# Kernel tuning notes

Hardware: AMD Instinct MI355X
Metric: run time of the kernel (lower is better)

## Reference

```python
import jax, jax.numpy as jnp
import numpy as np

EMBED = 2048
HQ = 32
HKV = 8
HD = EMBED // HQ          # 64
G = HQ // HKV             # 4 q heads per kv head
SCALE = 1.0 / np.sqrt(EMBED)  # module uses 1/sqrt(embed_dim), not head_dim
B, S = 4, 2048


def setup_inputs() -> dict:
    key = jax.random.key(0)
    ks = jax.random.split(key, 10)
    x = jax.random.normal(ks[0], (B, S, EMBED), dtype=jnp.float32)
    # RoPE tables: theta=10000, angles[t, i] = t / theta^(2i/HD)
    inv_freq = 1.0 / (10000.0 ** (jnp.arange(0, HD, 2, dtype=jnp.float32) / HD))  # [HD/2]
    angles = jnp.arange(S, dtype=jnp.float32)[:, None] * inv_freq[None, :]        # [S, HD/2]
    freqs_cos = jnp.cos(angles)
    freqs_sin = jnp.sin(angles)
    s = 0.02
    wq_w = jax.random.normal(ks[1], (EMBED, EMBED), jnp.float32) * s
    wq_b = jnp.zeros((EMBED,), jnp.float32)
    wk_w = jax.random.normal(ks[2], (HKV * HD, EMBED), jnp.float32) * s
    wk_b = jnp.zeros((HKV * HD,), jnp.float32)
    wv_w = jax.random.normal(ks[3], (HKV * HD, EMBED), jnp.float32) * s
    wv_b = jnp.zeros((HKV * HD,), jnp.float32)
    wo_w = jax.random.normal(ks[4], (EMBED, EMBED), jnp.float32) * s
    wo_b = jnp.zeros((EMBED,), jnp.float32)
    return dict(x=x, freqs_cos=freqs_cos, freqs_sin=freqs_sin,
                wq_w=wq_w, wq_b=wq_b, wk_w=wk_w, wk_b=wk_b,
                wv_w=wv_w, wv_b=wv_b, wo_w=wo_w, wo_b=wo_b)


def _rope(t, cos, sin):
    # t: [B, S, H, HD]; cos/sin: [S, HD/2] -> broadcast [1, S, 1, HD/2]
    tr = t[..., 0::2]
    ti = t[..., 1::2]
    c = cos[None, :, None, :]
    s = sin[None, :, None, :]
    out_r = tr * c - ti * s
    out_i = tr * s + ti * c
    # interleave back to [..., HD]
    return jnp.stack([out_r, out_i], axis=-1).reshape(t.shape)


def _forward(x, freqs_cos, freqs_sin, wq_w, wq_b, wk_w, wk_b, wv_w, wv_b, wo_w, wo_b):
    b, s, _ = x.shape
    q = (x @ wq_w.T + wq_b).reshape(b, s, HQ, HD)
    k = (x @ wk_w.T + wk_b).reshape(b, s, HKV, HD)
    v = (x @ wv_w.T + wv_b).reshape(b, s, HKV, HD)
    q = _rope(q, freqs_cos, freqs_sin)
    k = _rope(k, freqs_cos, freqs_sin)
    # GQA: group q heads as [HKV, G] instead of repeat_interleave'ing k/v
    qg = q.reshape(b, s, HKV, G, HD)
    scores = jnp.einsum('bqhgd,bkhd->bhgqk', qg, k) * SCALE  # [B,HKV,G,S,S]
    causal = jnp.tril(jnp.ones((s, s), dtype=bool))
    scores = jnp.where(causal, scores, jnp.finfo(scores.dtype).min)
    p = jax.nn.softmax(scores, axis=-1)
    o = jnp.einsum('bhgqk,bkhd->bqhgd', p, v).reshape(b, s, EMBED)
    return o @ wo_w.T + wo_b


def reference(x, freqs_cos, freqs_sin, wq_w, wq_b, wk_w, wk_b, wv_w, wv_b, wo_w, wo_b):
    return _forward(x, freqs_cos, freqs_sin, wq_w, wq_b, wk_w, wk_b,
                    wv_w, wv_b, wo_w, wo_b)
```

## Files before the change

### kernel.cpp

```cpp
#include <hip/hip_runtime.h>
#include <stdint.h>

typedef unsigned short u16;
typedef __attribute__((ext_vector_type(8))) short bf16x8;
typedef __attribute__((ext_vector_type(4))) float f32x4;

#define MFMA_BF16(a,b,c) __builtin_amdgcn_mfma_f32_16x16x32_bf16((a),(b),(c),0,0,0)

__device__ inline u16 f2bf(float f) {
  uint32_t u = __builtin_bit_cast(uint32_t, f);
  u = (u + 0x7FFFu + ((u >> 16) & 1u)) >> 16;
  return (u16)u;
}
__device__ inline float bf2f(u16 h) {
  uint32_t u = ((uint32_t)h) << 16;
  return __builtin_bit_cast(float, u);
}

__global__ __launch_bounds__(256) void cvt_kernel(const float* __restrict__ src,
                                                  u16* __restrict__ dst, int n4) {
  int i = blockIdx.x * 256 + threadIdx.x;
  if (i >= n4) return;
  float4 v = reinterpret_cast<const float4*>(src)[i];
  uint2 o;
  o.x = (uint32_t)f2bf(v.x) | ((uint32_t)f2bf(v.y) << 16);
  o.y = (uint32_t)f2bf(v.z) | ((uint32_t)f2bf(v.w) << 16);
  reinterpret_cast<uint2*>(dst)[i] = o;
}

template<typename OutT>
__global__ __launch_bounds__(256) void gemm_bt(
    const u16* __restrict__ A, const u16* __restrict__ B,
    const float* __restrict__ bias, OutT* __restrict__ C,
    int M, int N, int K)
{
  constexpr int LDT = 72;
  __shared__ u16 As[128 * LDT];
  __shared__ u16 Bs[128 * LDT];
  const int bm = blockIdx.y, bn = blockIdx.x;
  const int tid = threadIdx.x;
  const int lane = tid & 63;
  const int wv = tid >> 6;
  const int wm = wv >> 1, wn = wv & 1;
  const int g = lane >> 4, qn = lane & 15;

  f32x4 acc[4][4];
  #pragma unroll
  for (int i = 0; i < 4; ++i)
    #pragma unroll
    for (int j = 0; j < 4; ++j) acc[i][j] = (f32x4){0.f, 0.f, 0.f, 0.f};

  const u16* Ab = A + (size_t)bm * 128 * K;
  const u16* Bb = B + (size_t)bn * 128 * K;

  for (int kt = 0; kt < K; kt += 64) {
    __syncthreads();
    #pragma unroll
    for (int i = 0; i < 4; ++i) {
      int u = tid + 256 * i;
      int row = u >> 3, c = u & 7;
      uint4 va = *reinterpret_cast<const uint4*>(Ab + (size_t)row * K + kt + c * 8);
      *reinterpret_cast<uint4*>(As + row * LDT + c * 8) = va;
      uint4 vb = *reinterpret_cast<const uint4*>(Bb + (size_t)row * K + kt + c * 8);
      *reinterpret_cast<uint4*>(Bs + row * LDT + c * 8) = vb;
    }
    __syncthreads();
    #pragma unroll
    for (int ks = 0; ks < 2; ++ks) {
      bf16x8 af[4], bfr[4];
      #pragma unroll
      for (int mi = 0; mi < 4; ++mi)
        af[mi] = *reinterpret_cast<const bf16x8*>(As + (wm * 64 + mi * 16 + qn) * LDT + g * 8 + ks * 32);
      #pragma unroll
      for (int ni = 0; ni < 4; ++ni)
        bfr[ni] = *reinterpret_cast<const bf16x8*>(Bs + (wn * 64 + ni * 16 + qn) * LDT + g * 8 + ks * 32);
      #pragma unroll
      for (int mi = 0; mi < 4; ++mi)
        #pragma unroll
        for (int ni = 0; ni < 4; ++ni)
          acc[mi][ni] = MFMA_BF16(af[mi], bfr[ni], acc[mi][ni]);
    }
  }
  #pragma unroll
  for (int ni = 0; ni < 4; ++ni) {
    int col = bn * 128 + wn * 64 + ni * 16 + qn;
    float bs = bias[col];
    #pragma unroll
    for (int mi = 0; mi < 4; ++mi) {
      #pragma unroll
      for (int r = 0; r < 4; ++r) {
        int row = bm * 128 + wm * 64 + mi * 16 + g * 4 + r;
        float v = acc[mi][ni][r] + bs;
        if constexpr (sizeof(OutT) == 2) C[(size_t)row * N + col] = (OutT)f2bf(v);
        else                             C[(size_t)row * N + col] = v;
      }
    }
  }
}

__global__ __launch_bounds__(256) void rope_kernel(
    u16* __restrict__ T, const float* __restrict__ cosT, const float* __restrict__ sinT,
    int heads8, int n8)
{
  int i = blockIdx.x * 256 + threadIdx.x;
  if (i >= n8) return;
  int tok = i / heads8;
  int r = i - tok * heads8;
  int d0 = (r & 7) * 8;
  int s = tok & 2047;
  uint4 v = reinterpret_cast<uint4*>(T)[i];
  u16* e = reinterpret_cast<u16*>(&v);
  float4 c = *reinterpret_cast<const float4*>(cosT + s * 32 + d0 / 2);
  float4 sn = *reinterpret_cast<const float4*>(sinT + s * 32 + d0 / 2);
  float cc[4] = {c.x, c.y, c.z, c.w}, ss[4] = {sn.x, sn.y, sn.z, sn.w};
  #pragma unroll
  for (int j = 0; j < 4; ++j) {
    float tr = bf2f(e[2 * j]), ti = bf2f(e[2 * j + 1]);
    e[2 * j]     = f2bf(tr * cc[j] - ti * ss[j]);
    e[2 * j + 1] = f2bf(tr * ss[j] + ti * cc[j]);
  }
  reinterpret_cast<uint4*>(T)[i] = v;
}

__global__ __launch_bounds__(256) void attn_kernel(
    const u16* __restrict__ Q, const u16* __restrict__ Kb,
    const u16* __restrict__ Vb, u16* __restrict__ O)
{
  constexpr int LDK = 72;
  constexpr float SCALE = 0.02209708691207961f;
  __shared__ u16 Kl[64 * LDK];
  __shared__ u16 Vt[64 * LDK];
  __shared__ u16 Pl[4][16 * LDK];
  const int qt = blockIdx.x, hq = blockIdx.y, b = blockIdx.z;
  const int kvh = hq >> 2;
  const int tid = threadIdx.x, lane = tid & 63, w = tid >> 6;
  const int g = lane >> 4, qn = lane & 15;
  const int q_g = qt * 64 + w * 16 + qn;

  const u16* qrow = Q + ((size_t)(b * 2048 + q_g) * 2048 + hq * 64);
  bf16x8 qf[2];
  qf[0] = *reinterpret_cast<const bf16x8*>(qrow + g * 8);
  qf[1] = *reinterpret_cast<const bf16x8*>(qrow + g * 8 + 32);

  float m = -1e30f, l = 0.f;
  f32x4 oa[4];
  #pragma unroll
  for (int i = 0; i < 4; ++i) oa[i] = (f32x4){0.f, 0.f, 0.f, 0.f};

  const u16* Kbase = Kb + ((size_t)b * 2048 * 512 + kvh * 64);
  const u16* Vbase = Vb + ((size_t)b * 2048 * 512 + kvh * 64);

  const int nkt = qt + 1;
  for (int kt = 0; kt < nkt; ++kt) {
    __syncthreads();
    #pragma unroll
    for (int i = 0; i < 2; ++i) {
      int u = tid + 256 * i;
      int row = u >> 3, c = u & 7;
      uint4 v = *reinterpret_cast<const uint4*>(Kbase + (size_t)(kt * 64 + row) * 512 + c * 8);
      *reinterpret_cast<uint4*>(Kl + row * LDK + c * 8) = v;
    }
    #pragma unroll
    for (int i = 0; i < 2; ++i) {
      int u = tid + 256 * i;
      int rc = u >> 6, d = u & 63;
      uint4 pack;
      u16* tmp = reinterpret_cast<u16*>(&pack);
      #pragma unroll
      for (int j = 0; j < 8; ++j)
        tmp[j] = Vbase[(size_t)(kt * 64 + rc * 8 + j) * 512 + d];
      *reinterpret_cast<uint4*>(Vt + d * LDK + rc * 8) = pack;
    }
    __syncthreads();
    f32x4 st[4];
    #pragma unroll
    for (int cf = 0; cf < 4; ++cf) st[cf] = (f32x4){0.f, 0.f, 0.f, 0.f};
    #pragma unroll
    for (int ks = 0; ks < 2; ++ks) {
      #pragma unroll
      for (int cf = 0; cf < 4; ++cf) {
        bf16x8 kf = *reinterpret_cast<const bf16x8*>(Kl + (cf * 16 + qn) * LDK + g * 8 + ks * 32);
        st[cf] = MFMA_BF16(kf, qf[ks], st[cf]);
      }
    }
    float pv[16];
    float tmax = -1e30f;
    #pragma unroll
    for (int cf = 0; cf < 4; ++cf) {
      #pragma unroll
      for (int r = 0; r < 4; ++r) {
        int kp = kt * 64 + cf * 16 + g * 4 + r;
        float s = st[cf][r] * SCALE;
        if (kp > q_g) s = -1e30f;
        pv[cf * 4 + r] = s;
        tmax = fmaxf(tmax, s);
      }
    }
    tmax = fmaxf(tmax, __shfl_xor(tmax, 16));
    tmax = fmaxf(tmax, __shfl_xor(tmax, 32));
    float mnew = fmaxf(m, tmax);
    float fac = __expf(m - mnew);
    float lsum = 0.f;
    #pragma unroll
    for (int i = 0; i < 16; ++i) { float p = __expf(pv[i] - mnew); pv[i] = p; lsum += p; }
    lsum += __shfl_xor(lsum, 16);
    lsum += __shfl_xor(lsum, 32);
    l = l * fac + lsum;
    m = mnew;
    #pragma unroll
    for (int r = 0; r < 4; ++r) {
      float fr = __shfl(fac, (lane & 48) | (g * 4 + r));
      #pragma unroll
      for (int df = 0; df < 4; ++df) oa[df][r] *= fr;
    }
    u16* Pw = Pl[w];
    #pragma unroll
    for (int cf = 0; cf < 4; ++cf) {
      #pragma unroll
      for (int h = 0; h < 2; ++h) {
        uint32_t pk = (uint32_t)f2bf(pv[cf * 4 + 2 * h]) | ((uint32_t)f2bf(pv[cf * 4 + 2 * h + 1]) << 16);
        *reinterpret_cast<uint32_t*>(Pw + qn * LDK + cf * 16 + g * 4 + 2 * h) = pk;
      }
    }
    __syncthreads();
    #pragma unroll
    for (int ks = 0; ks < 2; ++ks) {
      bf16x8 pa = *reinterpret_cast<const bf16x8*>(Pw + qn * LDK + g * 8 + ks * 32);
      #pragma unroll
      for (int df = 0; df < 4; ++df) {
        bf16x8 vf = *reinterpret_cast<const bf16x8*>(Vt + (df * 16 + qn) * LDK + g * 8 + ks * 32);
        oa[df] = MFMA_BF16(pa, vf, oa[df]);
      }
    }
  }
  #pragma unroll
  for (int r = 0; r < 4; ++r) {
    float lr = __shfl(l, (lane & 48) | (g * 4 + r));
    float inv = 1.f / lr;
    int row_g = qt * 64 + w * 16 + g * 4 + r;
    u16* orow = O + ((size_t)(b * 2048 + row_g) * 2048 + hq * 64);
    #pragma unroll
    for (int df = 0; df < 4; ++df)
      orow[df * 16 + qn] = f2bf(oa[df][r] * inv);
  }
}

extern "C" void kernel_launch(void* const* d_in, const int* in_sizes, int n_in,
                              void* d_out, int out_size, void* d_ws, size_t ws_size,
                              hipStream_t stream) {
  const float* x    = (const float*)d_in[0];
  const float* fc   = (const float*)d_in[1];
  const float* fs   = (const float*)d_in[2];
  const float* wq_w = (const float*)d_in[3];
  const float* wq_b = (const float*)d_in[4];
  const float* wk_w = (const float*)d_in[5];
  const float* wk_b = (const float*)d_in[6];
  const float* wv_w = (const float*)d_in[7];
  const float* wv_b = (const float*)d_in[8];
  const float* wo_w = (const float*)d_in[9];
  const float* wo_b = (const float*)d_in[10];
  float* out = (float*)d_out;
  char* ws = (char*)d_ws;

  const size_t NEEDED = 96468992;
  if (ws_size < NEEDED) return;

  u16* x_bf  = (u16*)(ws);
  u16* Qb    = (u16*)(ws + 33554432);
  u16* Kb    = (u16*)(ws + 67108864);
  u16* Vb    = (u16*)(ws + 75497472);
  u16* Wbuf  = (u16*)(ws + 83886080);
  u16* wk_bf = (u16*)(ws + 92274688);
  u16* wv_bf = (u16*)(ws + 94371840);
  u16* Ob    = x_bf;

  cvt_kernel<<<16384, 256, 0, stream>>>(x,    x_bf, 4194304);
  cvt_kernel<<< 4096, 256, 0, stream>>>(wq_w, Wbuf, 1048576);
  cvt_kernel<<< 1024, 256, 0, stream>>>(wk_w, wk_bf, 262144);
  cvt_kernel<<< 1024, 256, 0, stream>>>(wv_w, wv_bf, 262144);

  gemm_bt<u16><<<dim3(16, 64), 256, 0, stream>>>(x_bf, Wbuf,  wq_b, Qb, 8192, 2048, 2048);
  gemm_bt<u16><<<dim3( 4, 64), 256, 0, stream>>>(x_bf, wk_bf, wk_b, Kb, 8192,  512, 2048);
  gemm_bt<u16><<<dim3( 4, 64), 256, 0, stream>>>(x_bf, wv_bf, wv_b, Vb, 8192,  512, 2048);

  cvt_kernel<<< 4096, 256, 0, stream>>>(wo_w, Wbuf, 1048576);

  rope_kernel<<<8192, 256, 0, stream>>>(Qb, fc, fs, 256, 2097152);
  rope_kernel<<<2048, 256, 0, stream>>>(Kb, fc, fs,  64,  524288);

  attn_kernel<<<dim3(32, 32, 4), 256, 0, stream>>>(Qb, Kb, Vb, Ob);

  gemm_bt<float><<<dim3(16, 64), 256, 0, stream>>>(Ob, Wbuf, wo_b, out, 8192, 2048, 2048);
}
```

Before: 773.1 us.

## Double-buffer attention K/V with async LDS loads, swizzling and causal tile skipping

The attention kernel now double-buffers K and V tiles. It prefetches the next tile with global_load_lds for K and register-staged loads for V while computing the current one, which removes one barrier per iteration. LDS padding is replaced by XOR swizzling, Q is prescaled by the softmax scale, and on the diagonal tile each wave skips fully masked column fragments. The GEMM also switches to direct global-to-LDS loads with an unpadded layout. That layout may cause LDS bank conflicts in the GEMM fragment reads, and prescaling Q in bf16 adds rounding error.

```diff
diff --git a/kernel.cpp b/kernel.cpp
--- a/kernel.cpp
+++ b/kernel.cpp
@@ -6,6 +6,10 @@
 typedef __attribute__((ext_vector_type(4))) float f32x4;
 
 #define MFMA_BF16(a,b,c) __builtin_amdgcn_mfma_f32_16x16x32_bf16((a),(b),(c),0,0,0)
+
+#define GLOAD_LDS16(g, l) \
+  __builtin_amdgcn_global_load_lds((const __attribute__((address_space(1))) void*)(g), \
+                                   (__attribute__((address_space(3))) void*)(l), 16, 0, 0)
 
 __device__ inline u16 f2bf(float f) {
   uint32_t u = __builtin_bit_cast(uint32_t, f);
@@ -34,9 +38,8 @@
     const float* __restrict__ bias, OutT* __restrict__ C,
     int M, int N, int K)
 {
-  constexpr int LDT = 72;
-  __shared__ u16 As[128 * LDT];
-  __shared__ u16 Bs[128 * LDT];
+  __shared__ u16 As[128 * 64];
+  __shared__ u16 Bs[128 * 64];
   const int bm = blockIdx.y, bn = blockIdx.x;
   const int tid = threadIdx.x;
   const int lane = tid & 63;
@@ -52,17 +55,16 @@
 
   const u16* Ab = A + (size_t)bm * 128 * K;
   const u16* Bb = B + (size_t)bn * 128 * K;
+  const int lr = lane >> 3, lc = lane & 7;
 
   for (int kt = 0; kt < K; kt += 64) {
     __syncthreads();
     #pragma unroll
     for (int i = 0; i < 4; ++i) {
-      int u = tid + 256 * i;
-      int row = u >> 3, c = u & 7;
-      uint4 va = *reinterpret_cast<const uint4*>(Ab + (size_t)row * K + kt + c * 8);
-      *reinterpret_cast<uint4*>(As + row * LDT + c * 8) = va;
-      uint4 vb = *reinterpret_cast<const uint4*>(Bb + (size_t)row * K + kt + c * 8);
-      *reinterpret_cast<uint4*>(Bs + row * LDT + c * 8) = vb;
+      int r0 = wv * 32 + i * 8;
+      size_t goff = (size_t)(r0 + lr) * K + kt + lc * 8;
+      GLOAD_LDS16(Ab + goff, As + r0 * 64);
+      GLOAD_LDS16(Bb + goff, Bs + r0 * 64);
     }
     __syncthreads();
     #pragma unroll
@@ -70,10 +72,10 @@
       bf16x8 af[4], bfr[4];
       #pragma unroll
       for (int mi = 0; mi < 4; ++mi)
-        af[mi] = *reinterpret_cast<const bf16x8*>(As + (wm * 64 + mi * 16 + qn) * LDT + g * 8 + ks * 32);
+        af[mi] = *reinterpret_cast<const bf16x8*>(As + (wm * 64 + mi * 16 + qn) * 64 + g * 8 + ks * 32);
       #pragma unroll
       for (int ni = 0; ni < 4; ++ni)
-        bfr[ni] = *reinterpret_cast<const bf16x8*>(Bs + (wn * 64 + ni * 16 + qn) * LDT + g * 8 + ks * 32);
+        bfr[ni] = *reinterpret_cast<const bf16x8*>(Bs + (wn * 64 + ni * 16 + qn) * 64 + g * 8 + ks * 32);
       #pragma unroll
       for (int mi = 0; mi < 4; ++mi)
         #pragma unroll
@@ -126,21 +128,30 @@
     const u16* __restrict__ Q, const u16* __restrict__ Kb,
     const u16* __restrict__ Vb, u16* __restrict__ O)
 {
-  constexpr int LDK = 72;
   constexpr float SCALE = 0.02209708691207961f;
-  __shared__ u16 Kl[64 * LDK];
-  __shared__ u16 Vt[64 * LDK];
-  __shared__ u16 Pl[4][16 * LDK];
+  __shared__ u16 Kl[2][64 * 64];
+  __shared__ u16 Vt[2][64 * 64];
+  __shared__ u16 Pl[4][16 * 64];
   const int qt = blockIdx.x, hq = blockIdx.y, b = blockIdx.z;
   const int kvh = hq >> 2;
   const int tid = threadIdx.x, lane = tid & 63, w = tid >> 6;
   const int g = lane >> 4, qn = lane & 15;
+  const int sw = qn & 7;
   const int q_g = qt * 64 + w * 16 + qn;
 
   const u16* qrow = Q + ((size_t)(b * 2048 + q_g) * 2048 + hq * 64);
   bf16x8 qf[2];
   qf[0] = *reinterpret_cast<const bf16x8*>(qrow + g * 8);
   qf[1] = *reinterpret_cast<const bf16x8*>(qrow + g * 8 + 32);
+  #pragma unroll
+  for (int i = 0; i < 2; ++i)
+    #pragma unroll
+    for (int j = 0; j < 8; ++j)
+      qf[i][j] = (short)f2bf(bf2f((u16)qf[i][j]) * SCALE);
+
+  bool dmask[4];
+  #pragma unroll
+  for (int r = 0; r < 4; ++r) dmask[r] = (g * 4 + r) > qn;
 
   float m = -1e30f, l = 0.f;
   f32x4 oa[4];
@@ -149,51 +160,83 @@
 
   const u16* Kbase = Kb + ((size_t)b * 2048 * 512 + kvh * 64);
   const u16* Vbase = Vb + ((size_t)b * 2048 * 512 + kvh * 64);
-
   const int nkt = qt + 1;
+  const int lr = lane >> 3, lc = lane & 7;
+  const int csw = lc ^ (lr & 7);
+
+  #pragma unroll
+  for (int i = 0; i < 2; ++i) {
+    int r0 = w * 16 + i * 8;
+    GLOAD_LDS16(Kbase + (size_t)(r0 + lr) * 512 + csw * 8, &Kl[0][r0 * 64]);
+  }
+  #pragma unroll
+  for (int i = 0; i < 2; ++i) {
+    int rc = w + 4 * i;
+    uint4 pk; u16* t = (u16*)&pk;
+    #pragma unroll
+    for (int j = 0; j < 8; ++j)
+      t[j] = Vbase[(size_t)(rc * 8 + j) * 512 + lane];
+    int slot = rc ^ (lane & 7);
+    *reinterpret_cast<uint4*>(&Vt[0][lane * 64 + slot * 8]) = pk;
+  }
+  __syncthreads();
+
+  int cur = 0;
   for (int kt = 0; kt < nkt; ++kt) {
-    __syncthreads();
-    #pragma unroll
-    for (int i = 0; i < 2; ++i) {
-      int u = tid + 256 * i;
-      int row = u >> 3, c = u & 7;
-      uint4 v = *reinterpret_cast<const uint4*>(Kbase + (size_t)(kt * 64 + row) * 512 + c * 8);
-      *reinterpret_cast<uint4*>(Kl + row * LDK + c * 8) = v;
-    }
-    #pragma unroll
-    for (int i = 0; i < 2; ++i) {
-      int u = tid + 256 * i;
-      int rc = u >> 6, d = u & 63;
-      uint4 pack;
-      u16* tmp = reinterpret_cast<u16*>(&pack);
-      #pragma unroll
-      for (int j = 0; j < 8; ++j)
-        tmp[j] = Vbase[(size_t)(kt * 64 + rc * 8 + j) * 512 + d];
-      *reinterpret_cast<uint4*>(Vt + d * LDK + rc * 8) = pack;
-    }
-    __syncthreads();
+    const bool haveNext = (kt + 1 < nkt);
+    const bool last = (kt == nkt - 1);
+    uint4 vr[2];
+    if (haveNext) {
+      #pragma unroll
+      for (int i = 0; i < 2; ++i) {
+        int r0 = w * 16 + i * 8;
+        GLOAD_LDS16(Kbase + (size_t)((kt + 1) * 64 + r0 + lr) * 512 + csw * 8,
+                    &Kl[cur ^ 1][r0 * 64]);
+      }
+      #pragma unroll
+      for (int i = 0; i < 2; ++i) {
+        int rc = w + 4 * i;
+        u16* t = (u16*)&vr[i];
+        #pragma unroll
+        for (int j = 0; j < 8; ++j)
+          t[j] = Vbase[(size_t)((kt + 1) * 64 + rc * 8 + j) * 512 + lane];
+      }
+    }
+
+    const u16* Kc = Kl[cur];
     f32x4 st[4];
     #pragma unroll
     for (int cf = 0; cf < 4; ++cf) st[cf] = (f32x4){0.f, 0.f, 0.f, 0.f};
     #pragma unroll
-    for (int ks = 0; ks < 2; ++ks) {
-      #pragma unroll
-      for (int cf = 0; cf < 4; ++cf) {
-        bf16x8 kf = *reinterpret_cast<const bf16x8*>(Kl + (cf * 16 + qn) * LDK + g * 8 + ks * 32);
+    for (int cf = 0; cf < 4; ++cf) {
+      if (last && cf > w) continue;
+      #pragma unroll
+      for (int ks = 0; ks < 2; ++ks) {
+        int slot = (g + 4 * ks) ^ sw;
+        bf16x8 kf = *reinterpret_cast<const bf16x8*>(Kc + (cf * 16 + qn) * 64 + slot * 8);
         st[cf] = MFMA_BF16(kf, qf[ks], st[cf]);
       }
     }
+
     float pv[16];
     float tmax = -1e30f;
     #pragma unroll
     for (int cf = 0; cf < 4; ++cf) {
-      #pragma unroll
-      for (int r = 0; r < 4; ++r) {
-        int kp = kt * 64 + cf * 16 + g * 4 + r;
-        float s = st[cf][r] * SCALE;
-        if (kp > q_g) s = -1e30f;
-        pv[cf * 4 + r] = s;
-        tmax = fmaxf(tmax, s);
+      if (last && cf > w) {
+        #pragma unroll
+        for (int r = 0; r < 4; ++r) pv[cf * 4 + r] = 0.f;
+      } else if (last && cf == w) {
+        #pragma unroll
+        for (int r = 0; r < 4; ++r) {
+          float s = dmask[r] ? -1e30f : st[cf][r];
+          pv[cf * 4 + r] = s; tmax = fmaxf(tmax, s);
+        }
+      } else {
+        #pragma unroll
+        for (int r = 0; r < 4; ++r) {
+          float s = st[cf][r];
+          pv[cf * 4 + r] = s; tmax = fmaxf(tmax, s);
+        }
       }
     }
     tmax = fmaxf(tmax, __shfl_xor(tmax, 16));
@@ -202,7 +245,14 @@
     float fac = __expf(m - mnew);
     float lsum = 0.f;
     #pragma unroll
-    for (int i = 0; i < 16; ++i) { float p = __expf(pv[i] - mnew); pv[i] = p; lsum += p; }
+    for (int cf = 0; cf < 4; ++cf) {
+      if (last && cf > w) continue;
+      #pragma unroll
+      for (int r = 0; r < 4; ++r) {
+        float p = __expf(pv[cf * 4 + r] - mnew);
+        pv[cf * 4 + r] = p; lsum += p;
+      }
+    }
     lsum += __shfl_xor(lsum, 16);
     lsum += __shfl_xor(lsum, 32);
     l = l * fac + lsum;
@@ -213,30 +263,45 @@
       #pragma unroll
       for (int df = 0; df < 4; ++df) oa[df][r] *= fr;
     }
+
     u16* Pw = Pl[w];
     #pragma unroll
     for (int cf = 0; cf < 4; ++cf) {
-      #pragma unroll
-      for (int h = 0; h < 2; ++h) {
-        uint32_t pk = (uint32_t)f2bf(pv[cf * 4 + 2 * h]) | ((uint32_t)f2bf(pv[cf * 4 + 2 * h + 1]) << 16);
-        *reinterpret_cast<uint32_t*>(Pw + qn * LDK + cf * 16 + g * 4 + 2 * h) = pk;
+      uint32_t lo = (uint32_t)f2bf(pv[cf * 4 + 0]) | ((uint32_t)f2bf(pv[cf * 4 + 1]) << 16);
+      uint32_t hi = (uint32_t)f2bf(pv[cf * 4 + 2]) | ((uint32_t)f2bf(pv[cf * 4 + 3]) << 16);
+      int slot = (2 * cf + (g >> 1)) ^ sw;
+      uint2 u2; u2.x = lo; u2.y = hi;
+      *reinterpret_cast<uint2*>(Pw + qn * 64 + slot * 8 + (g & 1) * 4) = u2;
+    }
+
+    if (haveNext) {
+      #pragma unroll
+      for (int i = 0; i < 2; ++i) {
+        int rc = w + 4 * i;
+        int slot = rc ^ (lane & 7);
+        *reinterpret_cast<uint4*>(&Vt[cur ^ 1][lane * 64 + slot * 8]) = vr[i];
+      }
+    }
+
+    const u16* Vc = Vt[cur];
+    #pragma unroll
+    for (int ks = 0; ks < 2; ++ks) {
+      int slotp = (g + 4 * ks) ^ sw;
+      bf16x8 pa = *reinterpret_cast<const bf16x8*>(Pw + qn * 64 + slotp * 8);
+      #pragma unroll
+      for (int df = 0; df < 4; ++df) {
+        bf16x8 vf = *reinterpret_cast<const bf16x8*>(Vc + (df * 16 + qn) * 64 + slotp * 8);
+        oa[df] = MFMA_BF16(pa, vf, oa[df]);
       }
     }
     __syncthreads();
-    #pragma unroll
-    for (int ks = 0; ks < 2; ++ks) {
-      bf16x8 pa = *reinterpret_cast<const bf16x8*>(Pw + qn * LDK + g * 8 + ks * 32);
-      #pragma unroll
-      for (int df = 0; df < 4; ++df) {
-        bf16x8 vf = *reinterpret_cast<const bf16x8*>(Vt + (df * 16 + qn) * LDK + g * 8 + ks * 32);
-        oa[df] = MFMA_BF16(pa, vf, oa[df]);
-      }
-    }
-  }
+    cur ^= 1;
+  }
+
   #pragma unroll
   for (int r = 0; r < 4; ++r) {
-    float lr = __shfl(l, (lane & 48) | (g * 4 + r));
-    float inv = 1.f / lr;
+    float lrv = __shfl(l, (lane & 48) | (g * 4 + r));
+    float inv = 1.f / lrv;
     int row_g = qt * 64 + w * 16 + g * 4 + r;
     u16* orow = O + ((size_t)(b * 2048 + row_g) * 2048 + hq * 64);
     #pragma unroll
```

Result: no change. 782.8 us (+1.3%).
